# Optimization experiments

Measured on AMD Instinct MI355X. Metric: run time of the kernel, lower is better.

Reference implementation:

```python
import jax, jax.numpy as jnp
import numpy as np

N, E, F_IN, H, F_OUT = 100000, 1600000, 128, 4, 16
NEG_SLOPE = 0.2


def setup_inputs() -> dict:
    key = jax.random.key(0)
    k1, k2, k3, k4, k5 = jax.random.split(key, 5)
    # xavier-ish scales
    s_w = (6.0 / (F_IN + H * F_OUT)) ** 0.5
    s_a = (6.0 / (1 + F_OUT)) ** 0.5
    return {
        "features": jax.random.normal(k1, (N, F_IN), dtype=jnp.float32),
        "edge_index": jax.random.randint(k2, (2, E), 0, N, dtype=jnp.int64),
        "weight_l": jax.random.uniform(k3, (F_IN, H * F_OUT), jnp.float32, -s_w, s_w),
        "weight_r": jax.random.uniform(k4, (F_IN, H * F_OUT), jnp.float32, -s_w, s_w),
        "att": jax.random.uniform(k5, (1, H, F_OUT), jnp.float32, -s_a, s_a),
        "bias": jnp.zeros((H * F_OUT,), dtype=jnp.float32),
    }


def reference(features, edge_index, weight_l, weight_r, att, bias):
    num_nodes = features.shape[0]
    src = edge_index[0]
    tgt = edge_index[1]
    h_l = (features @ weight_l).reshape(-1, H, F_OUT)  # [N,H,F]
    h_r = (features @ weight_r).reshape(-1, H, F_OUT)
    x_i = h_l[tgt]  # [E,H,F] gather target
    x_j = h_r[src]  # [E,H,F] gather source
    z = x_i + x_j
    z = jnp.where(z >= 0, z, NEG_SLOPE * z)  # leaky_relu
    scores = (z * att).sum(axis=-1)  # [E,H]
    # segment softmax keyed by target node
    m = jax.ops.segment_max(scores, tgt, num_segments=num_nodes)  # [N,H]
    ex = jnp.exp(scores - jax.lax.stop_gradient(m)[tgt])
    denom = jax.ops.segment_sum(ex, tgt, num_segments=num_nodes)  # [N,H]
    alpha = ex / denom[tgt]  # [E,H]
    messages = x_j * alpha[..., None]  # [E,H,F]
    out = jax.ops.segment_sum(messages, tgt, num_segments=num_nodes)  # [N,H,F]
    out = out.reshape(num_nodes, H * F_OUT) + bias
    return out
```

## Files before the change

### kernel.cpp

```cpp
#include <hip/hip_runtime.h>

#define NN 100000
#define NE 1600000
#define NB 782
#define CHUNK 8192
#define CAP 6144
#define LDP 136

typedef __attribute__((ext_vector_type(8))) short bf16x8;
typedef __attribute__((ext_vector_type(4))) float f32x4;

static __device__ __forceinline__ unsigned short f2bf(float f) {
  unsigned int u = __float_as_uint(f);
  u += 0x7fff + ((u >> 16) & 1);
  return (unsigned short)(u >> 16);
}

__global__ void wprep_k(const float* __restrict__ wl, const float* __restrict__ wr,
                        unsigned short* __restrict__ wt) {
  int i = blockIdx.x * 256 + threadIdx.x;
  int c = i >> 7, k = i & 127;
  float v = (c < 64) ? wl[k * 64 + c] : wr[k * 64 + (c - 64)];
  wt[i] = f2bf(v);
}

__global__ __launch_bounds__(256) void gemm_mfma(const float* __restrict__ feat,
                                                 const unsigned short* __restrict__ wt,
                                                 float* __restrict__ hl,
                                                 unsigned short* __restrict__ hrb) {
  __shared__ unsigned short ldsA[128][LDP];
  __shared__ unsigned short ldsB[128][LDP];
  const int tid = threadIdx.x;
  const int row0 = blockIdx.x * 128;

  for (int idx = tid; idx < 2048; idx += 256) {
    uint4 v = reinterpret_cast<const uint4*>(wt)[idx];
    *reinterpret_cast<uint4*>(&ldsB[idx >> 4][(idx & 15) * 8]) = v;
  }

  for (int it = 0; it < 16; ++it) {
    int r = it * 8 + (tid >> 5);
    int gr = row0 + r;
    int k4 = (tid & 31) * 4;
    float4 v = make_float4(0.f, 0.f, 0.f, 0.f);
    if (gr < NN) v = *reinterpret_cast<const float4*>(&feat[(size_t)gr * 128 + k4]);
    union { unsigned short s[4]; uint2 u; } pk;
    pk.s[0] = f2bf(v.x); pk.s[1] = f2bf(v.y); pk.s[2] = f2bf(v.z); pk.s[3] = f2bf(v.w);
    *reinterpret_cast<uint2*>(&ldsA[r][k4]) = pk.u;
  }
  __syncthreads();

  const int w  = tid >> 6;
  const int ln = tid & 63;
  const int lr = ln & 15;
  const int kb = (ln >> 4) * 8;

  f32x4 acc[2][8];
#pragma unroll
  for (int mt = 0; mt < 2; ++mt)
#pragma unroll
    for (int nt = 0; nt < 8; ++nt) acc[mt][nt] = (f32x4){0.f, 0.f, 0.f, 0.f};

#pragma unroll
  for (int t = 0; t < 4; ++t) {
    const int ko = t * 32 + kb;
    bf16x8 af0 = *reinterpret_cast<const bf16x8*>(&ldsA[w * 32 + lr][ko]);
    bf16x8 af1 = *reinterpret_cast<const bf16x8*>(&ldsA[w * 32 + 16 + lr][ko]);
    bf16x8 bfr[8];
#pragma unroll
    for (int nt = 0; nt < 8; ++nt)
      bfr[nt] = *reinterpret_cast<const bf16x8*>(&ldsB[nt * 16 + lr][ko]);
#pragma unroll
    for (int nt = 0; nt < 8; ++nt) {
      acc[0][nt] = __builtin_amdgcn_mfma_f32_16x16x32_bf16(af0, bfr[nt], acc[0][nt], 0, 0, 0);
      acc[1][nt] = __builtin_amdgcn_mfma_f32_16x16x32_bf16(af1, bfr[nt], acc[1][nt], 0, 0, 0);
    }
  }

#pragma unroll
  for (int mt = 0; mt < 2; ++mt) {
    int rrel = w * 32 + mt * 16 + (ln >> 4) * 4;
#pragma unroll
    for (int q = 0; q < 4; ++q) {
      int gr = row0 + rrel + q;
      if (gr < NN) {
#pragma unroll
        for (int nt = 0; nt < 4; ++nt)
          hl[(size_t)gr * 64 + nt * 16 + lr] = acc[mt][nt][q];
#pragma unroll
        for (int nt = 4; nt < 8; ++nt)
          hrb[(size_t)gr * 64 + (nt - 4) * 16 + lr] = f2bf(acc[mt][nt][q]);
      }
    }
  }
}

__global__ __launch_bounds__(256) void bhist_k(const int* __restrict__ tgt,
                                               int* __restrict__ bcnt) {
  __shared__ int lh[NB];
  const int tid = threadIdx.x;
  const int base = blockIdx.x * CHUNK;
  const int lim = min(CHUNK, NE - base);
  for (int b = tid; b < NB; b += 256) lh[b] = 0;
  __syncthreads();
  for (int i = tid; i < lim; i += 256)
    atomicAdd(&lh[tgt[base + i] >> 7], 1);
  __syncthreads();
  for (int b = tid; b < NB; b += 256)
    if (lh[b]) atomicAdd(&bcnt[b * 16], lh[b]);
}

__global__ __launch_bounds__(256) void bscan_k(const int* __restrict__ bcnt,
                                               int* __restrict__ bstart,
                                               int* __restrict__ bcursor) {
  __shared__ int sd[256];
  const int tid = threadIdx.x;
  int v[4]; int s = 0;
#pragma unroll
  for (int j = 0; j < 4; ++j) {
    int idx = tid * 4 + j;
    v[j] = (idx < NB) ? bcnt[idx * 16] : 0;
    s += v[j];
  }
  sd[tid] = s;
  __syncthreads();
  for (int off = 1; off < 256; off <<= 1) {
    int t = (tid >= off) ? sd[tid - off] : 0;
    __syncthreads();
    sd[tid] += t;
    __syncthreads();
  }
  int run = sd[tid] - s;
#pragma unroll
  for (int j = 0; j < 4; ++j) {
    int idx = tid * 4 + j;
    if (idx < NB) { bstart[idx] = run; bcursor[idx * 16] = run; }
    run += v[j];
  }
  if (tid == 255) bstart[NB] = NE;
}

__global__ __launch_bounds__(256) void bscatter_k(const int* __restrict__ edge,
                                                  int* __restrict__ bcursor,
                                                  int* __restrict__ brec) {
  __shared__ int lcnt[NB];
  __shared__ int lstart[NB];
  __shared__ int gbase[NB];
  __shared__ int lcur[NB];
  __shared__ int srec[CHUNK];
  __shared__ unsigned short bid[CHUNK];
  __shared__ int sd[256];
  const int tid = threadIdx.x;
  const int base = blockIdx.x * CHUNK;
  const int lim = min(CHUNK, NE - base);

  for (int b = tid; b < NB; b += 256) { lcnt[b] = 0; lcur[b] = 0; }
  __syncthreads();
  for (int i = tid; i < lim; i += 256)
    atomicAdd(&lcnt[edge[NE + base + i] >> 7], 1);
  __syncthreads();

  int v[4]; int s = 0;
#pragma unroll
  for (int j = 0; j < 4; ++j) {
    int idx = tid * 4 + j;
    v[j] = (idx < NB) ? lcnt[idx] : 0;
    s += v[j];
  }
  sd[tid] = s;
  __syncthreads();
  for (int off = 1; off < 256; off <<= 1) {
    int t = (tid >= off) ? sd[tid - off] : 0;
    __syncthreads();
    sd[tid] += t;
    __syncthreads();
  }
  int run = sd[tid] - s;
#pragma unroll
  for (int j = 0; j < 4; ++j) {
    int idx = tid * 4 + j;
    if (idx < NB) lstart[idx] = run;
    run += v[j];
  }
  __syncthreads();

  for (int b = tid; b < NB; b += 256)
    if (lcnt[b] > 0) gbase[b] = atomicAdd(&bcursor[b * 16], lcnt[b]);
  __syncthreads();

  for (int i = tid; i < lim; i += 256) {
    int tg = edge[NE + base + i];
    int sr = edge[base + i];
    int b = tg >> 7;
    int r = atomicAdd(&lcur[b], 1);
    int slot = lstart[b] + r;
    srec[slot] = (sr << 7) | (tg & 127);
    bid[slot] = (unsigned short)b;
  }
  __syncthreads();

  for (int i = tid; i < lim; i += 256) {
    int b = bid[i];
    brec[gbase[b] + i - lstart[b]] = srec[i];
  }
}

__global__ __launch_bounds__(256) void bsort_k(int* __restrict__ brec,
                                               const int* __restrict__ bstart,
                                               int* __restrict__ start) {
  __shared__ int srec[CAP];
  __shared__ int ncnt[128];
  __shared__ int nst[128];
  __shared__ int sd2[128];
  const int tid = threadIdx.x;
  const int b = blockIdx.x;
  const int s0 = bstart[b];
  const int cnt = bstart[b + 1] - s0;

  if (tid < 128) ncnt[tid] = 0;
  __syncthreads();
  for (int i = tid; i < cnt; i += 256) {
    int r = brec[s0 + i];
    srec[i] = r;
    atomicAdd(&ncnt[r & 127], 1);
  }
  __syncthreads();

  int val = (tid < 128) ? ncnt[tid] : 0;
  if (tid < 128) sd2[tid] = val;
  __syncthreads();
  for (int off = 1; off < 128; off <<= 1) {
    int t = 0;
    if (tid < 128 && tid >= off) t = sd2[tid - off];
    __syncthreads();
    if (tid < 128) sd2[tid] += t;
    __syncthreads();
  }
  if (tid < 128) {
    nst[tid] = sd2[tid] - val;
    int nid = (b << 7) + tid;
    if (nid < NN) start[nid] = s0 + nst[tid];
    ncnt[tid] = 0;
  }
  if (b == NB - 1 && tid == 0) start[NN] = NE;
  __syncthreads();

  for (int i = tid; i < cnt; i += 256) {
    int r = srec[i];
    int tl = r & 127;
    int p = atomicAdd(&ncnt[tl], 1);
    brec[s0 + nst[tl] + p] = r >> 7;
  }
}

__global__ __launch_bounds__(256) void node_k(const float* __restrict__ hl,
                                              const unsigned short* __restrict__ hrb,
                                              const int* __restrict__ ssrc,
                                              const int* __restrict__ start,
                                              const float* __restrict__ att,
                                              const float* __restrict__ bias,
                                              float* __restrict__ out) {
  const int lane = threadIdx.x & 63;
  const int n  = blockIdx.x * 4 + (threadIdx.x >> 6);
  const int g  = lane >> 4;
  const int fo = (lane & 15) * 4;

  const float4 xi = *reinterpret_cast<const float4*>(hl + (size_t)n * 64 + fo);
  const float4 a  = *reinterpret_cast<const float4*>(att + fo);
  const int s = start[n];
  const int e = start[n + 1];
  const unsigned short* __restrict__ hrp = hrb + fo;

  float  den = 0.f;
  float4 acc = make_float4(0.f, 0.f, 0.f, 0.f);

  for (int i = s; i < e; i += 8) {
    int r0 = i + g, r1 = i + 4 + g;
    bool v0 = r0 < e, v1 = r1 < e;
    int j0 = ssrc[v0 ? r0 : s];
    int j1 = ssrc[v1 ? r1 : s];
    uint2 p0 = *reinterpret_cast<const uint2*>(hrp + (size_t)j0 * 64);
    uint2 p1 = *reinterpret_cast<const uint2*>(hrp + (size_t)j1 * 64);
    float4 x0, x1;
    x0.x = __uint_as_float(p0.x << 16);
    x0.y = __uint_as_float(p0.x & 0xffff0000u);
    x0.z = __uint_as_float(p0.y << 16);
    x0.w = __uint_as_float(p0.y & 0xffff0000u);
    x1.x = __uint_as_float(p1.x << 16);
    x1.y = __uint_as_float(p1.x & 0xffff0000u);
    x1.z = __uint_as_float(p1.y << 16);
    x1.w = __uint_as_float(p1.y & 0xffff0000u);

    float4 z0, z1;
    z0.x = xi.x + x0.x; z0.y = xi.y + x0.y; z0.z = xi.z + x0.z; z0.w = xi.w + x0.w;
    z1.x = xi.x + x1.x; z1.y = xi.y + x1.y; z1.z = xi.z + x1.z; z1.w = xi.w + x1.w;
    z0.x = fmaxf(z0.x, 0.2f * z0.x); z0.y = fmaxf(z0.y, 0.2f * z0.y);
    z0.z = fmaxf(z0.z, 0.2f * z0.z); z0.w = fmaxf(z0.w, 0.2f * z0.w);
    z1.x = fmaxf(z1.x, 0.2f * z1.x); z1.y = fmaxf(z1.y, 0.2f * z1.y);
    z1.z = fmaxf(z1.z, 0.2f * z1.z); z1.w = fmaxf(z1.w, 0.2f * z1.w);

    float t0 = z0.x * a.x; t0 = fmaf(z0.y, a.y, t0);
    t0 = fmaf(z0.z, a.z, t0); t0 = fmaf(z0.w, a.w, t0);
    float t1 = z1.x * a.x; t1 = fmaf(z1.y, a.y, t1);
    t1 = fmaf(z1.z, a.z, t1); t1 = fmaf(z1.w, a.w, t1);

    t0 += __shfl_xor(t0, 1); t0 += __shfl_xor(t0, 2);
    t1 += __shfl_xor(t1, 1); t1 += __shfl_xor(t1, 2);

    float e0 = v0 ? __expf(t0) : 0.f;
    float e1 = v1 ? __expf(t1) : 0.f;
    den += e0 + e1;
    acc.x = fmaf(e0, x0.x, acc.x); acc.y = fmaf(e0, x0.y, acc.y);
    acc.z = fmaf(e0, x0.z, acc.z); acc.w = fmaf(e0, x0.w, acc.w);
    acc.x = fmaf(e1, x1.x, acc.x); acc.y = fmaf(e1, x1.y, acc.y);
    acc.z = fmaf(e1, x1.z, acc.z); acc.w = fmaf(e1, x1.w, acc.w);
  }

#pragma unroll
  for (int m = 16; m <= 32; m <<= 1) {
    den   += __shfl_xor(den, m);
    acc.x += __shfl_xor(acc.x, m);
    acc.y += __shfl_xor(acc.y, m);
    acc.z += __shfl_xor(acc.z, m);
    acc.w += __shfl_xor(acc.w, m);
  }

  if (g == 0) {
    float inv = (e > s) ? 1.f / den : 0.f;
    float4 b4 = *reinterpret_cast<const float4*>(bias + fo);
    float4 r;
    r.x = fmaf(acc.x, inv, b4.x);
    r.y = fmaf(acc.y, inv, b4.y);
    r.z = fmaf(acc.z, inv, b4.z);
    r.w = fmaf(acc.w, inv, b4.w);
    *reinterpret_cast<float4*>(out + (size_t)n * 64 + fo) = r;
  }
}

extern "C" void kernel_launch(void* const* d_in, const int* in_sizes, int n_in,
                              void* d_out, int out_size, void* d_ws, size_t ws_size,
                              hipStream_t stream) {
  const float* feat = (const float*)d_in[0];
  const int*   edge = (const int*)d_in[1];
  const float* wl   = (const float*)d_in[2];
  const float* wr   = (const float*)d_in[3];
  const float* att  = (const float*)d_in[4];
  const float* bias = (const float*)d_in[5];
  float* out = (float*)d_out;

  float* hl       = (float*)d_ws;
  unsigned short* hrb = (unsigned short*)(hl + (size_t)NN * 64);
  int*   brec     = (int*)(hrb + (size_t)NN * 64);
  int*   bcnt     = brec + NE;
  int*   bstart   = bcnt + NB * 16;
  int*   bcursor  = bstart + NB + 1;
  int*   start    = bcursor + NB * 16;
  unsigned short* wt = (unsigned short*)(start + NN + 1);

  (void)hipMemsetAsync(bcnt, 0, NB * 16 * sizeof(int), stream);

  const int nchunk = (NE + CHUNK - 1) / CHUNK;
  wprep_k<<<64, 256, 0, stream>>>(wl, wr, wt);
  gemm_mfma<<<(NN + 127) / 128, 256, 0, stream>>>(feat, wt, hl, hrb);
  bhist_k<<<nchunk, 256, 0, stream>>>(edge + NE, bcnt);
  bscan_k<<<1, 256, 0, stream>>>(bcnt, bstart, bcursor);
  bscatter_k<<<nchunk, 256, 0, stream>>>(edge, bcursor, brec);
  bsort_k<<<NB, 256, 0, stream>>>(brec, bstart, start);
  node_k<<<NN / 4, 256, 0, stream>>>(hl, hrb, brec, start, att, bias, out);
}
```

Baseline: 247.6 us.

## Load GEMM operands directly from global memory into MFMA fragments, skip LDS staging

```diff
diff --git a/kernel.cpp b/kernel.cpp
--- a/kernel.cpp
+++ b/kernel.cpp
@@ -3,9 +3,8 @@
 #define NN 100000
 #define NE 1600000
 #define NB 782
-#define CHUNK 8192
+#define CHUNK 4096
 #define CAP 6144
-#define LDP 136
 
 typedef __attribute__((ext_vector_type(8))) short bf16x8;
 typedef __attribute__((ext_vector_type(4))) float f32x4;
@@ -14,6 +13,13 @@
   unsigned int u = __float_as_uint(f);
   u += 0x7fff + ((u >> 16) & 1);
   return (unsigned short)(u >> 16);
+}
+
+static __device__ __forceinline__ bf16x8 cvt8(float4 lo, float4 hi) {
+  union { unsigned short s[8]; bf16x8 v; } u;
+  u.s[0] = f2bf(lo.x); u.s[1] = f2bf(lo.y); u.s[2] = f2bf(lo.z); u.s[3] = f2bf(lo.w);
+  u.s[4] = f2bf(hi.x); u.s[5] = f2bf(hi.y); u.s[6] = f2bf(hi.z); u.s[7] = f2bf(hi.w);
+  return u.v;
 }
 
 __global__ void wprep_k(const float* __restrict__ wl, const float* __restrict__ wr,
@@ -28,33 +34,18 @@
                                                  const unsigned short* __restrict__ wt,
                                                  float* __restrict__ hl,
                                                  unsigned short* __restrict__ hrb) {
-  __shared__ unsigned short ldsA[128][LDP];
-  __shared__ unsigned short ldsB[128][LDP];
   const int tid = threadIdx.x;
   const int row0 = blockIdx.x * 128;
-
-  for (int idx = tid; idx < 2048; idx += 256) {
-    uint4 v = reinterpret_cast<const uint4*>(wt)[idx];
-    *reinterpret_cast<uint4*>(&ldsB[idx >> 4][(idx & 15) * 8]) = v;
-  }
-
-  for (int it = 0; it < 16; ++it) {
-    int r = it * 8 + (tid >> 5);
-    int gr = row0 + r;
-    int k4 = (tid & 31) * 4;
-    float4 v = make_float4(0.f, 0.f, 0.f, 0.f);
-    if (gr < NN) v = *reinterpret_cast<const float4*>(&feat[(size_t)gr * 128 + k4]);
-    union { unsigned short s[4]; uint2 u; } pk;
-    pk.s[0] = f2bf(v.x); pk.s[1] = f2bf(v.y); pk.s[2] = f2bf(v.z); pk.s[3] = f2bf(v.w);
-    *reinterpret_cast<uint2*>(&ldsA[r][k4]) = pk.u;
-  }
-  __syncthreads();
-
   const int w  = tid >> 6;
   const int ln = tid & 63;
   const int lr = ln & 15;
   const int kb = (ln >> 4) * 8;
 
+  const int r0g = row0 + w * 32 + lr;
+  const int r1g = r0g + 16;
+  const bool ok0 = r0g < NN, ok1 = r1g < NN;
+  const float4 zero4 = make_float4(0.f, 0.f, 0.f, 0.f);
+
   f32x4 acc[2][8];
 #pragma unroll
   for (int mt = 0; mt < 2; ++mt)
@@ -64,12 +55,16 @@
 #pragma unroll
   for (int t = 0; t < 4; ++t) {
     const int ko = t * 32 + kb;
-    bf16x8 af0 = *reinterpret_cast<const bf16x8*>(&ldsA[w * 32 + lr][ko]);
-    bf16x8 af1 = *reinterpret_cast<const bf16x8*>(&ldsA[w * 32 + 16 + lr][ko]);
+    float4 a0l = ok0 ? *reinterpret_cast<const float4*>(&feat[(size_t)r0g * 128 + ko]) : zero4;
+    float4 a0h = ok0 ? *reinterpret_cast<const float4*>(&feat[(size_t)r0g * 128 + ko + 4]) : zero4;
+    float4 a1l = ok1 ? *reinterpret_cast<const float4*>(&feat[(size_t)r1g * 128 + ko]) : zero4;
+    float4 a1h = ok1 ? *reinterpret_cast<const float4*>(&feat[(size_t)r1g * 128 + ko + 4]) : zero4;
+    bf16x8 af0 = cvt8(a0l, a0h);
+    bf16x8 af1 = cvt8(a1l, a1h);
     bf16x8 bfr[8];
 #pragma unroll
     for (int nt = 0; nt < 8; ++nt)
-      bfr[nt] = *reinterpret_cast<const bf16x8*>(&ldsB[nt * 16 + lr][ko]);
+      bfr[nt] = *reinterpret_cast<const bf16x8*>(&wt[(size_t)(nt * 16 + lr) * 128 + ko]);
 #pragma unroll
     for (int nt = 0; nt < 8; ++nt) {
       acc[0][nt] = __builtin_amdgcn_mfma_f32_16x16x32_bf16(af0, bfr[nt], acc[0][nt], 0, 0, 0);
```

After: 270.4 us. 1.09x slower.

## Remap node kernel lanes so each lane owns one head across 16 edges

Applied to the files above, without the earlier changes.

```diff
diff --git a/kernel.cpp b/kernel.cpp
--- a/kernel.cpp
+++ b/kernel.cpp
@@ -3,7 +3,7 @@
 #define NN 100000
 #define NE 1600000
 #define NB 782
-#define CHUNK 8192
+#define CHUNK 4096
 #define CAP 6144
 #define LDP 136
 
@@ -253,6 +253,30 @@
   }
 }
 
+#define UNPK(D_, U0_, U1_)                             \
+  D_.x = __uint_as_float((U0_) << 16);                 \
+  D_.y = __uint_as_float((U0_) & 0xffff0000u);         \
+  D_.z = __uint_as_float((U1_) << 16);                 \
+  D_.w = __uint_as_float((U1_) & 0xffff0000u);
+
+#define LKY(Z_, XI_, X_)                                          \
+  Z_.x = XI_.x + X_.x; Z_.y = XI_.y + X_.y;                       \
+  Z_.z = XI_.z + X_.z; Z_.w = XI_.w + X_.w;                       \
+  Z_.x = fmaxf(Z_.x, 0.2f * Z_.x); Z_.y = fmaxf(Z_.y, 0.2f * Z_.y); \
+  Z_.z = fmaxf(Z_.z, 0.2f * Z_.z); Z_.w = fmaxf(Z_.w, 0.2f * Z_.w);
+
+#define DOT(T_, Z_, A_)                                \
+  T_ = fmaf(Z_.x, A_.x, T_); T_ = fmaf(Z_.y, A_.y, T_); \
+  T_ = fmaf(Z_.z, A_.z, T_); T_ = fmaf(Z_.w, A_.w, T_);
+
+#define ACC(AC_, E_, X_)                               \
+  AC_.x = fmaf(E_, X_.x, AC_.x); AC_.y = fmaf(E_, X_.y, AC_.y); \
+  AC_.z = fmaf(E_, X_.z, AC_.z); AC_.w = fmaf(E_, X_.w, AC_.w);
+
+#define RED(V_, M_)                                    \
+  V_.x += __shfl_xor(V_.x, M_); V_.y += __shfl_xor(V_.y, M_); \
+  V_.z += __shfl_xor(V_.z, M_); V_.w += __shfl_xor(V_.w, M_);
+
 __global__ __launch_bounds__(256) void node_k(const float* __restrict__ hl,
                                               const unsigned short* __restrict__ hrb,
                                               const int* __restrict__ ssrc,
@@ -262,78 +286,67 @@
                                               float* __restrict__ out) {
   const int lane = threadIdx.x & 63;
   const int n  = blockIdx.x * 4 + (threadIdx.x >> 6);
-  const int g  = lane >> 4;
-  const int fo = (lane & 15) * 4;
-
-  const float4 xi = *reinterpret_cast<const float4*>(hl + (size_t)n * 64 + fo);
-  const float4 a  = *reinterpret_cast<const float4*>(att + fo);
+  const int g  = lane >> 2;
+  const int h  = lane & 3;
+  const int ho = h * 16;
+
+  const float4* xiq = reinterpret_cast<const float4*>(hl + (size_t)n * 64 + ho);
+  const float4 xi0 = xiq[0], xi1 = xiq[1], xi2 = xiq[2], xi3 = xiq[3];
+  const float4* aq = reinterpret_cast<const float4*>(att + ho);
+  const float4 a0 = aq[0], a1 = aq[1], a2 = aq[2], a3 = aq[3];
+
   const int s = start[n];
   const int e = start[n + 1];
-  const unsigned short* __restrict__ hrp = hrb + fo;
+  const unsigned short* __restrict__ hrp = hrb + ho;
 
   float  den = 0.f;
-  float4 acc = make_float4(0.f, 0.f, 0.f, 0.f);
-
-  for (int i = s; i < e; i += 8) {
-    int r0 = i + g, r1 = i + 4 + g;
-    bool v0 = r0 < e, v1 = r1 < e;
-    int j0 = ssrc[v0 ? r0 : s];
-    int j1 = ssrc[v1 ? r1 : s];
-    uint2 p0 = *reinterpret_cast<const uint2*>(hrp + (size_t)j0 * 64);
-    uint2 p1 = *reinterpret_cast<const uint2*>(hrp + (size_t)j1 * 64);
-    float4 x0, x1;
-    x0.x = __uint_as_float(p0.x << 16);
-    x0.y = __uint_as_float(p0.x & 0xffff0000u);
-    x0.z = __uint_as_float(p0.y << 16);
-    x0.w = __uint_as_float(p0.y & 0xffff0000u);
-    x1.x = __uint_as_float(p1.x << 16);
-    x1.y = __uint_as_float(p1.x & 0xffff0000u);
-    x1.z = __uint_as_float(p1.y << 16);
-    x1.w = __uint_as_float(p1.y & 0xffff0000u);
-
-    float4 z0, z1;
-    z0.x = xi.x + x0.x; z0.y = xi.y + x0.y; z0.z = xi.z + x0.z; z0.w = xi.w + x0.w;
-    z1.x = xi.x + x1.x; z1.y = xi.y + x1.y; z1.z = xi.z + x1.z; z1.w = xi.w + x1.w;
-    z0.x = fmaxf(z0.x, 0.2f * z0.x); z0.y = fmaxf(z0.y, 0.2f * z0.y);
-    z0.z = fmaxf(z0.z, 0.2f * z0.z); z0.w = fmaxf(z0.w, 0.2f * z0.w);
-    z1.x = fmaxf(z1.x, 0.2f * z1.x); z1.y = fmaxf(z1.y, 0.2f * z1.y);
-    z1.z = fmaxf(z1.z, 0.2f * z1.z); z1.w = fmaxf(z1.w, 0.2f * z1.w);
-
-    float t0 = z0.x * a.x; t0 = fmaf(z0.y, a.y, t0);
-    t0 = fmaf(z0.z, a.z, t0); t0 = fmaf(z0.w, a.w, t0);
-    float t1 = z1.x * a.x; t1 = fmaf(z1.y, a.y, t1);
-    t1 = fmaf(z1.z, a.z, t1); t1 = fmaf(z1.w, a.w, t1);
-
-    t0 += __shfl_xor(t0, 1); t0 += __shfl_xor(t0, 2);
-    t1 += __shfl_xor(t1, 1); t1 += __shfl_xor(t1, 2);
-
-    float e0 = v0 ? __expf(t0) : 0.f;
-    float e1 = v1 ? __expf(t1) : 0.f;
-    den += e0 + e1;
-    acc.x = fmaf(e0, x0.x, acc.x); acc.y = fmaf(e0, x0.y, acc.y);
-    acc.z = fmaf(e0, x0.z, acc.z); acc.w = fmaf(e0, x0.w, acc.w);
-    acc.x = fmaf(e1, x1.x, acc.x); acc.y = fmaf(e1, x1.y, acc.y);
-    acc.z = fmaf(e1, x1.z, acc.z); acc.w = fmaf(e1, x1.w, acc.w);
-  }
-
-#pragma unroll
-  for (int m = 16; m <= 32; m <<= 1) {
-    den   += __shfl_xor(den, m);
-    acc.x += __shfl_xor(acc.x, m);
-    acc.y += __shfl_xor(acc.y, m);
-    acc.z += __shfl_xor(acc.z, m);
-    acc.w += __shfl_xor(acc.w, m);
+  float4 acc0 = make_float4(0.f, 0.f, 0.f, 0.f);
+  float4 acc1 = acc0, acc2 = acc0, acc3 = acc0;
+
+  for (int i = s; i < e; i += 16) {
+    int r = i + g;
+    bool valid = r < e;
+    int j = ssrc[valid ? r : s];
+    const uint4* p = reinterpret_cast<const uint4*>(hrp + (size_t)j * 64);
+    uint4 q0 = p[0];
+    uint4 q1 = p[1];
+
+    float4 x0, x1, x2, x3;
+    UNPK(x0, q0.x, q0.y); UNPK(x1, q0.z, q0.w);
+    UNPK(x2, q1.x, q1.y); UNPK(x3, q1.z, q1.w);
+
+    float4 z;
+    float t = 0.f;
+    LKY(z, xi0, x0); DOT(t, z, a0);
+    LKY(z, xi1, x1); DOT(t, z, a1);
+    LKY(z, xi2, x2); DOT(t, z, a2);
+    LKY(z, xi3, x3); DOT(t, z, a3);
+
+    float ex = valid ? __expf(t) : 0.f;
+    den += ex;
+    ACC(acc0, ex, x0); ACC(acc1, ex, x1);
+    ACC(acc2, ex, x2); ACC(acc3, ex, x3);
+  }
+
+#pragma unroll
+  for (int m = 4; m <= 32; m <<= 1) {
+    den += __shfl_xor(den, m);
+    RED(acc0, m); RED(acc1, m); RED(acc2, m); RED(acc3, m);
   }
 
   if (g == 0) {
     float inv = (e > s) ? 1.f / den : 0.f;
-    float4 b4 = *reinterpret_cast<const float4*>(bias + fo);
-    float4 r;
-    r.x = fmaf(acc.x, inv, b4.x);
-    r.y = fmaf(acc.y, inv, b4.y);
-    r.z = fmaf(acc.z, inv, b4.z);
-    r.w = fmaf(acc.w, inv, b4.w);
-    *reinterpret_cast<float4*>(out + (size_t)n * 64 + fo) = r;
+    const float4* bq = reinterpret_cast<const float4*>(bias + ho);
+    float4* oq = reinterpret_cast<float4*>(out + (size_t)n * 64 + ho);
+    float4 b, r;
+    b = bq[0]; r.x = fmaf(acc0.x, inv, b.x); r.y = fmaf(acc0.y, inv, b.y);
+    r.z = fmaf(acc0.z, inv, b.z); r.w = fmaf(acc0.w, inv, b.w); oq[0] = r;
+    b = bq[1]; r.x = fmaf(acc1.x, inv, b.x); r.y = fmaf(acc1.y, inv, b.y);
+    r.z = fmaf(acc1.z, inv, b.z); r.w = fmaf(acc1.w, inv, b.w); oq[1] = r;
+    b = bq[2]; r.x = fmaf(acc2.x, inv, b.x); r.y = fmaf(acc2.y, inv, b.y);
+    r.z = fmaf(acc2.z, inv, b.z); r.w = fmaf(acc2.w, inv, b.w); oq[2] = r;
+    b = bq[3]; r.x = fmaf(acc3.x, inv, b.x); r.y = fmaf(acc3.y, inv, b.y);
+    r.z = fmaf(acc3.z, inv, b.z); r.w = fmaf(acc3.w, inv, b.w); oq[3] = r;
   }
 }
 
```

Result: slower. 297.0 us (+20.0%).

## Replace histogram+scan with fixed-capacity bucket slots and unroll edge gather loop

Applied to the files above, without the earlier changes.

```diff
diff --git a/kernel.cpp b/kernel.cpp
--- a/kernel.cpp
+++ b/kernel.cpp
@@ -3,8 +3,8 @@
 #define NN 100000
 #define NE 1600000
 #define NB 782
-#define CHUNK 8192
-#define CAP 6144
+#define CHUNK 4096
+#define BCAP 2560
 #define LDP 136
 
 typedef __attribute__((ext_vector_type(8))) short bf16x8;
@@ -17,11 +17,12 @@
 }
 
 __global__ void wprep_k(const float* __restrict__ wl, const float* __restrict__ wr,
-                        unsigned short* __restrict__ wt) {
+                        unsigned short* __restrict__ wt, int* __restrict__ bcursor) {
   int i = blockIdx.x * 256 + threadIdx.x;
   int c = i >> 7, k = i & 127;
   float v = (c < 64) ? wl[k * 64 + c] : wr[k * 64 + (c - 64)];
   wt[i] = f2bf(v);
+  if (i < NB) bcursor[i * 16] = i * BCAP;
 }
 
 __global__ __launch_bounds__(256) void gemm_mfma(const float* __restrict__ feat,
@@ -93,51 +94,6 @@
       }
     }
   }
-}
-
-__global__ __launch_bounds__(256) void bhist_k(const int* __restrict__ tgt,
-                                               int* __restrict__ bcnt) {
-  __shared__ int lh[NB];
-  const int tid = threadIdx.x;
-  const int base = blockIdx.x * CHUNK;
-  const int lim = min(CHUNK, NE - base);
-  for (int b = tid; b < NB; b += 256) lh[b] = 0;
-  __syncthreads();
-  for (int i = tid; i < lim; i += 256)
-    atomicAdd(&lh[tgt[base + i] >> 7], 1);
-  __syncthreads();
-  for (int b = tid; b < NB; b += 256)
-    if (lh[b]) atomicAdd(&bcnt[b * 16], lh[b]);
-}
-
-__global__ __launch_bounds__(256) void bscan_k(const int* __restrict__ bcnt,
-                                               int* __restrict__ bstart,
-                                               int* __restrict__ bcursor) {
-  __shared__ int sd[256];
-  const int tid = threadIdx.x;
-  int v[4]; int s = 0;
-#pragma unroll
-  for (int j = 0; j < 4; ++j) {
-    int idx = tid * 4 + j;
-    v[j] = (idx < NB) ? bcnt[idx * 16] : 0;
-    s += v[j];
-  }
-  sd[tid] = s;
-  __syncthreads();
-  for (int off = 1; off < 256; off <<= 1) {
-    int t = (tid >= off) ? sd[tid - off] : 0;
-    __syncthreads();
-    sd[tid] += t;
-    __syncthreads();
-  }
-  int run = sd[tid] - s;
-#pragma unroll
-  for (int j = 0; j < 4; ++j) {
-    int idx = tid * 4 + j;
-    if (idx < NB) { bstart[idx] = run; bcursor[idx * 16] = run; }
-    run += v[j];
-  }
-  if (tid == 255) bstart[NB] = NE;
 }
 
 __global__ __launch_bounds__(256) void bscatter_k(const int* __restrict__ edge,
@@ -206,16 +162,16 @@
 }
 
 __global__ __launch_bounds__(256) void bsort_k(int* __restrict__ brec,
-                                               const int* __restrict__ bstart,
-                                               int* __restrict__ start) {
-  __shared__ int srec[CAP];
+                                               const int* __restrict__ bcursor,
+                                               int2* __restrict__ srange) {
+  __shared__ int srec[BCAP];
   __shared__ int ncnt[128];
   __shared__ int nst[128];
   __shared__ int sd2[128];
   const int tid = threadIdx.x;
   const int b = blockIdx.x;
-  const int s0 = bstart[b];
-  const int cnt = bstart[b + 1] - s0;
+  const int s0 = b * BCAP;
+  const int cnt = bcursor[b * 16] - s0;
 
   if (tid < 128) ncnt[tid] = 0;
   __syncthreads();
@@ -237,12 +193,12 @@
     __syncthreads();
   }
   if (tid < 128) {
-    nst[tid] = sd2[tid] - val;
+    int st = sd2[tid] - val;
+    nst[tid] = st;
     int nid = (b << 7) + tid;
-    if (nid < NN) start[nid] = s0 + nst[tid];
+    if (nid < NN) srange[nid] = make_int2(s0 + st, s0 + st + val);
     ncnt[tid] = 0;
   }
-  if (b == NB - 1 && tid == 0) start[NN] = NE;
   __syncthreads();
 
   for (int i = tid; i < cnt; i += 256) {
@@ -253,10 +209,20 @@
   }
 }
 
+#define UNPK(D_, U0_, U1_)                             \
+  D_.x = __uint_as_float((U0_) << 16);                 \
+  D_.y = __uint_as_float((U0_) & 0xffff0000u);         \
+  D_.z = __uint_as_float((U1_) << 16);                 \
+  D_.w = __uint_as_float((U1_) & 0xffff0000u);
+
+#define ACC(AC_, E_, X_)                               \
+  AC_.x = fmaf(E_, X_.x, AC_.x); AC_.y = fmaf(E_, X_.y, AC_.y); \
+  AC_.z = fmaf(E_, X_.z, AC_.z); AC_.w = fmaf(E_, X_.w, AC_.w);
+
 __global__ __launch_bounds__(256) void node_k(const float* __restrict__ hl,
                                               const unsigned short* __restrict__ hrb,
                                               const int* __restrict__ ssrc,
-                                              const int* __restrict__ start,
+                                              const int2* __restrict__ srange,
                                               const float* __restrict__ att,
                                               const float* __restrict__ bias,
                                               float* __restrict__ out) {
@@ -267,53 +233,38 @@
 
   const float4 xi = *reinterpret_cast<const float4*>(hl + (size_t)n * 64 + fo);
   const float4 a  = *reinterpret_cast<const float4*>(att + fo);
-  const int s = start[n];
-  const int e = start[n + 1];
+  const int2 se = srange[n];
+  const int s = se.x, e = se.y;
   const unsigned short* __restrict__ hrp = hrb + fo;
 
   float  den = 0.f;
   float4 acc = make_float4(0.f, 0.f, 0.f, 0.f);
 
-  for (int i = s; i < e; i += 8) {
-    int r0 = i + g, r1 = i + 4 + g;
-    bool v0 = r0 < e, v1 = r1 < e;
-    int j0 = ssrc[v0 ? r0 : s];
-    int j1 = ssrc[v1 ? r1 : s];
-    uint2 p0 = *reinterpret_cast<const uint2*>(hrp + (size_t)j0 * 64);
-    uint2 p1 = *reinterpret_cast<const uint2*>(hrp + (size_t)j1 * 64);
-    float4 x0, x1;
-    x0.x = __uint_as_float(p0.x << 16);
-    x0.y = __uint_as_float(p0.x & 0xffff0000u);
-    x0.z = __uint_as_float(p0.y << 16);
-    x0.w = __uint_as_float(p0.y & 0xffff0000u);
-    x1.x = __uint_as_float(p1.x << 16);
-    x1.y = __uint_as_float(p1.x & 0xffff0000u);
-    x1.z = __uint_as_float(p1.y << 16);
-    x1.w = __uint_as_float(p1.y & 0xffff0000u);
-
-    float4 z0, z1;
-    z0.x = xi.x + x0.x; z0.y = xi.y + x0.y; z0.z = xi.z + x0.z; z0.w = xi.w + x0.w;
-    z1.x = xi.x + x1.x; z1.y = xi.y + x1.y; z1.z = xi.z + x1.z; z1.w = xi.w + x1.w;
-    z0.x = fmaxf(z0.x, 0.2f * z0.x); z0.y = fmaxf(z0.y, 0.2f * z0.y);
-    z0.z = fmaxf(z0.z, 0.2f * z0.z); z0.w = fmaxf(z0.w, 0.2f * z0.w);
-    z1.x = fmaxf(z1.x, 0.2f * z1.x); z1.y = fmaxf(z1.y, 0.2f * z1.y);
-    z1.z = fmaxf(z1.z, 0.2f * z1.z); z1.w = fmaxf(z1.w, 0.2f * z1.w);
-
-    float t0 = z0.x * a.x; t0 = fmaf(z0.y, a.y, t0);
-    t0 = fmaf(z0.z, a.z, t0); t0 = fmaf(z0.w, a.w, t0);
-    float t1 = z1.x * a.x; t1 = fmaf(z1.y, a.y, t1);
-    t1 = fmaf(z1.z, a.z, t1); t1 = fmaf(z1.w, a.w, t1);
-
-    t0 += __shfl_xor(t0, 1); t0 += __shfl_xor(t0, 2);
-    t1 += __shfl_xor(t1, 1); t1 += __shfl_xor(t1, 2);
-
-    float e0 = v0 ? __expf(t0) : 0.f;
-    float e1 = v1 ? __expf(t1) : 0.f;
-    den += e0 + e1;
-    acc.x = fmaf(e0, x0.x, acc.x); acc.y = fmaf(e0, x0.y, acc.y);
-    acc.z = fmaf(e0, x0.z, acc.z); acc.w = fmaf(e0, x0.w, acc.w);
-    acc.x = fmaf(e1, x1.x, acc.x); acc.y = fmaf(e1, x1.y, acc.y);
-    acc.z = fmaf(e1, x1.z, acc.z); acc.w = fmaf(e1, x1.w, acc.w);
+  for (int i = s; i < e; i += 16) {
+    uint2 p[4];
+    bool  v[4];
+#pragma unroll
+    for (int u = 0; u < 4; ++u) {
+      int r = i + u * 4 + g;
+      v[u] = r < e;
+      int j = ssrc[v[u] ? r : s];
+      p[u] = *reinterpret_cast<const uint2*>(hrp + (size_t)j * 64);
+    }
+#pragma unroll
+    for (int u = 0; u < 4; ++u) {
+      float4 x;
+      UNPK(x, p[u].x, p[u].y);
+      float4 z;
+      z.x = xi.x + x.x; z.y = xi.y + x.y; z.z = xi.z + x.z; z.w = xi.w + x.w;
+      z.x = fmaxf(z.x, 0.2f * z.x); z.y = fmaxf(z.y, 0.2f * z.y);
+      z.z = fmaxf(z.z, 0.2f * z.z); z.w = fmaxf(z.w, 0.2f * z.w);
+      float t = z.x * a.x;
+      t = fmaf(z.y, a.y, t); t = fmaf(z.z, a.z, t); t = fmaf(z.w, a.w, t);
+      t += __shfl_xor(t, 1); t += __shfl_xor(t, 2);
+      float ex = v[u] ? __expf(t) : 0.f;
+      den += ex;
+      ACC(acc, ex, x);
+    }
   }
 
 #pragma unroll
@@ -351,20 +302,14 @@
   float* hl       = (float*)d_ws;
   unsigned short* hrb = (unsigned short*)(hl + (size_t)NN * 64);
   int*   brec     = (int*)(hrb + (size_t)NN * 64);
-  int*   bcnt     = brec + NE;
-  int*   bstart   = bcnt + NB * 16;
-  int*   bcursor  = bstart + NB + 1;
-  int*   start    = bcursor + NB * 16;
-  unsigned short* wt = (unsigned short*)(start + NN + 1);
-
-  (void)hipMemsetAsync(bcnt, 0, NB * 16 * sizeof(int), stream);
+  int*   bcursor  = brec + (size_t)NB * BCAP;
+  int2*  srange   = (int2*)(bcursor + NB * 16);
+  unsigned short* wt = (unsigned short*)(srange + NN);
 
   const int nchunk = (NE + CHUNK - 1) / CHUNK;
-  wprep_k<<<64, 256, 0, stream>>>(wl, wr, wt);
+  wprep_k<<<64, 256, 0, stream>>>(wl, wr, wt, bcursor);
   gemm_mfma<<<(NN + 127) / 128, 256, 0, stream>>>(feat, wt, hl, hrb);
-  bhist_k<<<nchunk, 256, 0, stream>>>(edge + NE, bcnt);
-  bscan_k<<<1, 256, 0, stream>>>(bcnt, bstart, bcursor);
   bscatter_k<<<nchunk, 256, 0, stream>>>(edge, bcursor, brec);
-  bsort_k<<<NB, 256, 0, stream>>>(brec, bstart, start);
-  node_k<<<NN / 4, 256, 0, stream>>>(hl, hrb, brec, start, att, bias, out);
-}
+  bsort_k<<<NB, 256, 0, stream>>>(brec, bcursor, srange);
+  node_k<<<NN / 4, 256, 0, stream>>>(hl, hrb, brec, srange, att, bias, out);
+}
```

Result: faster. 223.2 us (-9.8%).
